# Kernel optimization log

Hardware: AMD Instinct MI355X
Metric: run time of the kernel (lower is better)

Reference implementation:

```python
import jax, jax.numpy as jnp
import numpy as np

B, T, D, H = 8, 8192, 1024, 16
HD = D // H  # head_dim = 64


def setup_inputs() -> dict:
    key = jax.random.key(0)
    ks = jax.random.split(key, 6)
    x = jax.random.normal(ks[0], (B, D), jnp.float32)
    past_k = jax.random.normal(ks[1], (B, T, H, HD), jnp.float32)
    past_v = jax.random.normal(ks[2], (B, T, H, HD), jnp.float32)
    idx = jax.random.randint(ks[3], (B,), 0, T)
    W_attn = jax.random.normal(ks[4], (D, 3 * D), jnp.float32) * 0.02
    b_attn = jnp.zeros((3 * D,), jnp.float32)
    W_proj = jax.random.normal(ks[5], (D, D), jnp.float32) * 0.02
    b_proj = jnp.zeros((D,), jnp.float32)
    return dict(x=x, past_k=past_k, past_v=past_v, idx=idx,
                W_attn=W_attn, b_attn=b_attn, W_proj=W_proj, b_proj=b_proj)


def reference(x, past_k, past_v, idx, W_attn, b_attn, W_proj, b_proj):
    # fused qkv projection: [B, 3D]
    qkv = x @ W_attn + b_attn
    q, k, v = jnp.split(qkv, 3, axis=-1)
    q = q.reshape(B, 1, H, HD)          # q_len = 1 (decode step)
    k_step = k.reshape(B, H, HD)
    v_step = v.reshape(B, H, HD)
    # one-hot scatter update of KV cache at position idx (as in original)
    oh = jax.nn.one_hot(idx, T, dtype=x.dtype)[:, :, None, None]  # [B,T,1,1]
    k_all = past_k * (1.0 - oh) + oh * k_step[:, None]            # [B,T,H,HD]
    v_all = past_v * (1.0 - oh) + oh * v_step[:, None]
    # causal mask over cache: positions <= idx are valid
    mask = jnp.arange(T) <= idx[:, None]                          # [B,T]
    scale = 1.0 / jnp.sqrt(jnp.asarray(HD, x.dtype))
    scores = jnp.einsum('bqhd,bkhd->bhqk', q * scale, k_all)      # [B,H,1,T]
    big_neg = jnp.finfo(scores.dtype).min
    scores = jnp.where(mask[:, None, None, :], scores, big_neg)
    attn = jax.nn.softmax(scores, axis=-1)
    y = jnp.einsum('bhqk,bkhd->bqhd', attn, v_all).reshape(B, D)
    y = y @ W_proj + b_proj
    return (y, k_step, v_step)
```

## Files before the change

kernel.cpp:

```cpp
#include <hip/hip_runtime.h>
#include <hip/hip_bf16.h>

#define BB 8
#define TT 8192
#define HH 16
#define HDIM 64
#define DDIM 1024
#define NS 16
#define TSPLIT 512
#define KS1 16
#define KS2 32

__device__ __forceinline__ int load_idx(const int* __restrict__ idx, int b) {
  const bool wide = (idx[1] == 0) && (idx[3] == 0) && (idx[5] == 0) && (idx[7] == 0);
  int v = wide ? idx[2 * b] : idx[b];
  return min(max(v, 0), TT - 1);
}

__global__ __launch_bounds__(256) void qkv_split_kernel(
    const float* __restrict__ x, const float* __restrict__ W,
    float* __restrict__ part)
{
  const int bid = blockIdx.x;
  const int ks = bid & (KS1 - 1);
  const int jc = (bid >> 4) % 3;
  const int b  = bid / (3 * KS1);
  const int tid = threadIdx.x;

  __shared__ float x_s[64];
  if (tid < 64) x_s[tid] = x[b * DDIM + ks * 64 + tid];
  __syncthreads();

  const int j0 = jc * 1024 + tid * 4;
  const float* wp = W + (size_t)(ks * 64) * 3072 + j0;
  float4 acc = {0.f, 0.f, 0.f, 0.f};
  #pragma unroll 8
  for (int dd = 0; dd < 64; ++dd) {
    float4 w4 = *(const float4*)(wp + (size_t)dd * 3072);
    const float xv = x_s[dd];
    acc.x += xv * w4.x; acc.y += xv * w4.y;
    acc.z += xv * w4.z; acc.w += xv * w4.w;
  }
  *(float4*)(part + (size_t)ks * (BB * 3072) + b * 3072 + j0) = acc;
}

__global__ __launch_bounds__(256) void qkv_reduce_kernel(
    const float* __restrict__ part, const float* __restrict__ bias,
    float* __restrict__ q_ws, float* __restrict__ kstep_ws,
    float* __restrict__ vstep_ws, float* __restrict__ out)
{
  const int g = blockIdx.x * 256 + threadIdx.x;
  const int b = g / 3072;
  const int j = g % 3072;
  float acc = bias[j];
  #pragma unroll
  for (int ks = 0; ks < KS1; ++ks) acc += part[(size_t)ks * (BB * 3072) + g];

  if (j < 1024) {
    q_ws[b * DDIM + j] = acc * 0.125f;
  } else if (j < 2048) {
    const int jj = j - 1024;
    kstep_ws[b * DDIM + jj] = acc;
    out[8192 + b * DDIM + jj] = acc;
  } else {
    const int jj = j - 2048;
    vstep_ws[b * DDIM + jj] = acc;
    out[16384 + b * DDIM + jj] = acc;
  }
}

__global__ __launch_bounds__(256) void attn_partial_kernel(
    const float* __restrict__ past_k, const float* __restrict__ past_v,
    const int* __restrict__ idx,
    const float* __restrict__ q_ws, const float* __restrict__ kstep_ws,
    const float* __restrict__ vstep_ws,
    float* __restrict__ part_m, float* __restrict__ part_l,
    float* __restrict__ part_o)
{
  const int tid = threadIdx.x;
  const int s  = blockIdx.x & (NS - 1);
  const int h  = (blockIdx.x >> 4) & (HH - 1);
  const int b  = blockIdx.x >> 8;
  const int idxb = load_idx(idx, b);
  const int t0 = s * TSPLIT;
  const int bhs = (b * HH + h) * NS + s;

  if (t0 > idxb) {
    if (tid == 0) { part_m[bhs] = -1e30f; part_l[bhs] = 0.f; }
    return;
  }
  const int nvalid = min(TSPLIT, idxb - t0 + 1);

  __shared__ float q_s[HDIM];
  __shared__ float p_s[TSPLIT];
  __shared__ float redm[8], redl[8];
  __shared__ float o_s[16 * HDIM];

  if (tid < HDIM) q_s[tid] = q_ws[b * DDIM + h * HDIM + tid];
  __syncthreads();

  const float* Kb = past_k + (((size_t)b * TT + t0) * HH + h) * HDIM;
  const float* krow_step = kstep_ws + b * DDIM + h * HDIM;
  float sc[2];
  #pragma unroll
  for (int i = 0; i < 2; ++i) {
    const int tl = tid + i * 256;
    float v = -1e30f;
    if (tl < nvalid) {
      const float* kr = (t0 + tl == idxb) ? krow_step
                                          : (Kb + (size_t)tl * (HH * HDIM));
      const float4* k4 = (const float4*)kr;
      float a0 = 0.f, a1 = 0.f, a2 = 0.f, a3 = 0.f;
      #pragma unroll
      for (int seg = 0; seg < 16; ++seg) {
        float4 u = k4[seg];
        a0 += q_s[seg * 4 + 0] * u.x;
        a1 += q_s[seg * 4 + 1] * u.y;
        a2 += q_s[seg * 4 + 2] * u.z;
        a3 += q_s[seg * 4 + 3] * u.w;
      }
      v = (a0 + a1) + (a2 + a3);
    }
    sc[i] = v;
  }

  float lmax = fmaxf(sc[0], sc[1]);
  #pragma unroll
  for (int m = 32; m > 0; m >>= 1) lmax = fmaxf(lmax, __shfl_xor(lmax, m, 64));
  if ((tid & 63) == 0) redm[tid >> 6] = lmax;
  __syncthreads();
  const float mh = fmaxf(fmaxf(redm[0], redm[1]), fmaxf(redm[2], redm[3]));

  float lsum = 0.f;
  #pragma unroll
  for (int i = 0; i < 2; ++i) {
    float p = __expf(sc[i] - mh);
    p_s[tid + i * 256] = p;
    lsum += p;
  }
  #pragma unroll
  for (int m = 32; m > 0; m >>= 1) lsum += __shfl_xor(lsum, m, 64);
  if ((tid & 63) == 0) redl[tid >> 6] = lsum;
  __syncthreads();
  if (tid == 0) {
    part_m[bhs] = mh;
    part_l[bhs] = redl[0] + redl[1] + redl[2] + redl[3];
  }

  const int tg = tid >> 4;
  const int d0 = (tid & 15) * 4;
  const float* Vb = past_v + (((size_t)b * TT + t0) * HH + h) * HDIM + d0;
  const float* vrow_step = vstep_ws + b * DDIM + h * HDIM + d0;
  float a0 = 0.f, a1 = 0.f, a2 = 0.f, a3 = 0.f;
  for (int tl = tg; tl < nvalid; tl += 16) {
    const float p = p_s[tl];
    const float4 u = *(const float4*)((t0 + tl == idxb)
                                          ? vrow_step
                                          : (Vb + (size_t)tl * (HH * HDIM)));
    a0 += p * u.x; a1 += p * u.y; a2 += p * u.z; a3 += p * u.w;
  }
  o_s[tg * HDIM + d0 + 0] = a0;
  o_s[tg * HDIM + d0 + 1] = a1;
  o_s[tg * HDIM + d0 + 2] = a2;
  o_s[tg * HDIM + d0 + 3] = a3;
  __syncthreads();
  if (tid < HDIM) {
    float acc = 0.f;
    #pragma unroll
    for (int g2 = 0; g2 < 16; ++g2) acc += o_s[g2 * HDIM + tid];
    part_o[(size_t)bhs * HDIM + tid] = acc;
  }
}

__global__ __launch_bounds__(64) void attn_combine_kernel(
    const float* __restrict__ part_m, const float* __restrict__ part_l,
    const float* __restrict__ part_o, float* __restrict__ y_ws)
{
  const int bh = blockIdx.x;
  const int lane = threadIdx.x;

  float m[NS], l[NS];
  float M = -1e30f;
  #pragma unroll
  for (int s = 0; s < NS; ++s) {
    m[s] = part_m[bh * NS + s];
    l[s] = part_l[bh * NS + s];
    M = fmaxf(M, m[s]);
  }
  float L = 0.f, acc = 0.f;
  #pragma unroll
  for (int s = 0; s < NS; ++s) {
    float w = (l[s] > 0.f) ? __expf(m[s] - M) : 0.f;
    if (w > 0.f) {
      L += l[s] * w;
      acc += w * part_o[(size_t)(bh * NS + s) * HDIM + lane];
    }
  }
  y_ws[bh * HDIM + lane] = (L > 0.f) ? (acc / L) : 0.f;
}

__global__ __launch_bounds__(256) void proj_split_kernel(
    const float* __restrict__ y_ws, const float* __restrict__ W,
    float* __restrict__ part)
{
  const int bid = blockIdx.x;
  const int ks = bid & (KS2 - 1);
  const int b  = bid >> 5;
  const int tid = threadIdx.x;

  __shared__ float y_s[32];
  if (tid < 32) y_s[tid] = y_ws[b * DDIM + ks * 32 + tid];
  __syncthreads();

  const int j0 = tid * 4;
  const float* wp = W + (size_t)(ks * 32) * DDIM + j0;
  float4 acc = {0.f, 0.f, 0.f, 0.f};
  #pragma unroll 8
  for (int dd = 0; dd < 32; ++dd) {
    float4 w4 = *(const float4*)(wp + (size_t)dd * DDIM);
    const float yv = y_s[dd];
    acc.x += yv * w4.x; acc.y += yv * w4.y;
    acc.z += yv * w4.z; acc.w += yv * w4.w;
  }
  *(float4*)(part + (size_t)ks * (BB * DDIM) + b * DDIM + j0) = acc;
}

__global__ __launch_bounds__(256) void proj_reduce_kernel(
    const float* __restrict__ part, const float* __restrict__ bias,
    float* __restrict__ out)
{
  const int g = blockIdx.x * 256 + threadIdx.x;
  const int j = g & 1023;
  float acc = bias[j];
  #pragma unroll
  for (int ks = 0; ks < KS2; ++ks) acc += part[(size_t)ks * (BB * DDIM) + g];
  out[g] = acc;
}

extern "C" void kernel_launch(void* const* d_in, const int* in_sizes, int n_in,
                              void* d_out, int out_size, void* d_ws, size_t ws_size,
                              hipStream_t stream) {
  const float* x      = (const float*)d_in[0];
  const float* past_k = (const float*)d_in[1];
  const float* past_v = (const float*)d_in[2];
  const int*   idx    = (const int*)  d_in[3];
  const float* W_attn = (const float*)d_in[4];
  const float* b_attn = (const float*)d_in[5];
  const float* W_proj = (const float*)d_in[6];
  const float* b_proj = (const float*)d_in[7];
  float* out = (float*)d_out;

  float* ws        = (float*)d_ws;
  float* q_ws      = ws;
  float* kstep_ws  = ws + 8192;
  float* vstep_ws  = ws + 16384;
  float* y_ws      = ws + 24576;
  float* part_m    = ws + 32768;
  float* part_l    = ws + 34816;
  float* part_o    = ws + 36864;
  float* qkv_part  = ws + 167936;
  float* proj_part = ws + 561152;

  qkv_split_kernel<<<dim3(BB * 3 * KS1), dim3(256), 0, stream>>>(
      x, W_attn, qkv_part);
  qkv_reduce_kernel<<<dim3(96), dim3(256), 0, stream>>>(
      qkv_part, b_attn, q_ws, kstep_ws, vstep_ws, out);
  attn_partial_kernel<<<dim3(BB * HH * NS), dim3(256), 0, stream>>>(
      past_k, past_v, idx, q_ws, kstep_ws, vstep_ws, part_m, part_l, part_o);
  attn_combine_kernel<<<dim3(BB * HH), dim3(64), 0, stream>>>(
      part_m, part_l, part_o, y_ws);
  proj_split_kernel<<<dim3(BB * KS2), dim3(256), 0, stream>>>(
      y_ws, W_proj, proj_part);
  proj_reduce_kernel<<<dim3(32), dim3(256), 0, stream>>>(
      proj_part, b_proj, out);
}
```

Baseline: 540.2 us.

## Coalesce K dot-products across lanes, fuse attention combine into projection, double QKV split

The score computation now gives four lanes to each key row, each loading interleaved float4 chunks, and reduces them with lane shuffles. This makes global K reads more coalesced than the previous one-row-per-thread pattern. The separate attention-combine kernel is removed and its log-sum-exp merge is recomputed inside the projection split kernel, saving one launch at the cost of redundant combine work across blocks. The QKV split factor is doubled so more blocks read W_attn in parallel, which doubles the partial-sum traffic in the reduce kernel.

```diff
diff --git a/kernel.cpp b/kernel.cpp
--- a/kernel.cpp
+++ b/kernel.cpp
@@ -8,7 +8,7 @@
 #define DDIM 1024
 #define NS 16
 #define TSPLIT 512
-#define KS1 16
+#define KS1 32
 #define KS2 32
 
 __device__ __forceinline__ int load_idx(const int* __restrict__ idx, int b) {
@@ -23,19 +23,19 @@
 {
   const int bid = blockIdx.x;
   const int ks = bid & (KS1 - 1);
-  const int jc = (bid >> 4) % 3;
+  const int jc = (bid >> 5) % 3;
   const int b  = bid / (3 * KS1);
   const int tid = threadIdx.x;
 
-  __shared__ float x_s[64];
-  if (tid < 64) x_s[tid] = x[b * DDIM + ks * 64 + tid];
+  __shared__ float x_s[32];
+  if (tid < 32) x_s[tid] = x[b * DDIM + ks * 32 + tid];
   __syncthreads();
 
   const int j0 = jc * 1024 + tid * 4;
-  const float* wp = W + (size_t)(ks * 64) * 3072 + j0;
+  const float* wp = W + (size_t)(ks * 32) * 3072 + j0;
   float4 acc = {0.f, 0.f, 0.f, 0.f};
   #pragma unroll 8
-  for (int dd = 0; dd < 64; ++dd) {
+  for (int dd = 0; dd < 32; ++dd) {
     float4 w4 = *(const float4*)(wp + (size_t)dd * 3072);
     const float xv = x_s[dd];
     acc.x += xv * w4.x; acc.y += xv * w4.y;
@@ -101,43 +101,50 @@
 
   const float* Kb = past_k + (((size_t)b * TT + t0) * HH + h) * HDIM;
   const float* krow_step = kstep_ws + b * DDIM + h * HDIM;
-  float sc[2];
-  #pragma unroll
-  for (int i = 0; i < 2; ++i) {
-    const int tl = tid + i * 256;
-    float v = -1e30f;
-    if (tl < nvalid) {
-      const float* kr = (t0 + tl == idxb) ? krow_step
-                                          : (Kb + (size_t)tl * (HH * HDIM));
+  const int rowg = tid >> 2;
+  const int li   = tid & 3;
+  #pragma unroll
+  for (int r = 0; r < 8; ++r) {
+    const int row = rowg + r * 64;
+    float a = 0.f;
+    if (row < nvalid) {
+      const float* kr = (t0 + row == idxb)
+                            ? krow_step
+                            : (Kb + (size_t)row * (HH * HDIM));
       const float4* k4 = (const float4*)kr;
       float a0 = 0.f, a1 = 0.f, a2 = 0.f, a3 = 0.f;
       #pragma unroll
-      for (int seg = 0; seg < 16; ++seg) {
-        float4 u = k4[seg];
-        a0 += q_s[seg * 4 + 0] * u.x;
-        a1 += q_s[seg * 4 + 1] * u.y;
-        a2 += q_s[seg * 4 + 2] * u.z;
-        a3 += q_s[seg * 4 + 3] * u.w;
+      for (int i = 0; i < 4; ++i) {
+        const int q4 = li + i * 4;
+        float4 u = k4[q4];
+        const int d = q4 * 4;
+        a0 += q_s[d + 0] * u.x;
+        a1 += q_s[d + 1] * u.y;
+        a2 += q_s[d + 2] * u.z;
+        a3 += q_s[d + 3] * u.w;
       }
-      v = (a0 + a1) + (a2 + a3);
+      a = (a0 + a1) + (a2 + a3);
     }
-    sc[i] = v;
-  }
-
-  float lmax = fmaxf(sc[0], sc[1]);
+    a += __shfl_xor(a, 1, 64);
+    a += __shfl_xor(a, 2, 64);
+    if (li == 0) p_s[row] = (row < nvalid) ? a : -1e30f;
+  }
+  __syncthreads();
+
+  const float s0 = p_s[tid];
+  const float s1 = p_s[tid + 256];
+  float lmax = fmaxf(s0, s1);
   #pragma unroll
   for (int m = 32; m > 0; m >>= 1) lmax = fmaxf(lmax, __shfl_xor(lmax, m, 64));
   if ((tid & 63) == 0) redm[tid >> 6] = lmax;
   __syncthreads();
   const float mh = fmaxf(fmaxf(redm[0], redm[1]), fmaxf(redm[2], redm[3]));
 
-  float lsum = 0.f;
-  #pragma unroll
-  for (int i = 0; i < 2; ++i) {
-    float p = __expf(sc[i] - mh);
-    p_s[tid + i * 256] = p;
-    lsum += p;
-  }
+  const float p0 = __expf(s0 - mh);
+  const float p1 = __expf(s1 - mh);
+  p_s[tid] = p0;
+  p_s[tid + 256] = p1;
+  float lsum = p0 + p1;
   #pragma unroll
   for (int m = 32; m > 0; m >>= 1) lsum += __shfl_xor(lsum, m, 64);
   if ((tid & 63) == 0) redl[tid >> 6] = lsum;
@@ -172,36 +179,10 @@
   }
 }
 
-__global__ __launch_bounds__(64) void attn_combine_kernel(
+__global__ __launch_bounds__(256) void proj_split_kernel(
     const float* __restrict__ part_m, const float* __restrict__ part_l,
-    const float* __restrict__ part_o, float* __restrict__ y_ws)
-{
-  const int bh = blockIdx.x;
-  const int lane = threadIdx.x;
-
-  float m[NS], l[NS];
-  float M = -1e30f;
-  #pragma unroll
-  for (int s = 0; s < NS; ++s) {
-    m[s] = part_m[bh * NS + s];
-    l[s] = part_l[bh * NS + s];
-    M = fmaxf(M, m[s]);
-  }
-  float L = 0.f, acc = 0.f;
-  #pragma unroll
-  for (int s = 0; s < NS; ++s) {
-    float w = (l[s] > 0.f) ? __expf(m[s] - M) : 0.f;
-    if (w > 0.f) {
-      L += l[s] * w;
-      acc += w * part_o[(size_t)(bh * NS + s) * HDIM + lane];
-    }
-  }
-  y_ws[bh * HDIM + lane] = (L > 0.f) ? (acc / L) : 0.f;
-}
-
-__global__ __launch_bounds__(256) void proj_split_kernel(
-    const float* __restrict__ y_ws, const float* __restrict__ W,
-    float* __restrict__ part)
+    const float* __restrict__ part_o,
+    const float* __restrict__ W, float* __restrict__ part)
 {
   const int bid = blockIdx.x;
   const int ks = bid & (KS2 - 1);
@@ -209,7 +190,29 @@
   const int tid = threadIdx.x;
 
   __shared__ float y_s[32];
-  if (tid < 32) y_s[tid] = y_ws[b * DDIM + ks * 32 + tid];
+  if (tid < 32) {
+    const int h = ks >> 1;
+    const int d = (ks & 1) * 32 + tid;
+    const int bh = b * HH + h;
+    float m[NS], l[NS];
+    float M = -1e30f;
+    #pragma unroll
+    for (int s = 0; s < NS; ++s) {
+      m[s] = part_m[bh * NS + s];
+      l[s] = part_l[bh * NS + s];
+      M = fmaxf(M, m[s]);
+    }
+    float L = 0.f, acc = 0.f;
+    #pragma unroll
+    for (int s = 0; s < NS; ++s) {
+      float w = (l[s] > 0.f) ? __expf(m[s] - M) : 0.f;
+      if (w > 0.f) {
+        L += l[s] * w;
+        acc += w * part_o[(size_t)(bh * NS + s) * HDIM + d];
+      }
+    }
+    y_s[tid] = (L > 0.f) ? (acc / L) : 0.f;
+  }
   __syncthreads();
 
   const int j0 = tid * 4;
@@ -254,12 +257,11 @@
   float* q_ws      = ws;
   float* kstep_ws  = ws + 8192;
   float* vstep_ws  = ws + 16384;
-  float* y_ws      = ws + 24576;
-  float* part_m    = ws + 32768;
-  float* part_l    = ws + 34816;
-  float* part_o    = ws + 36864;
-  float* qkv_part  = ws + 167936;
-  float* proj_part = ws + 561152;
+  float* part_m    = ws + 24576;
+  float* part_l    = ws + 26624;
+  float* part_o    = ws + 28672;
+  float* qkv_part  = ws + 159744;
+  float* proj_part = ws + 946176;
 
   qkv_split_kernel<<<dim3(BB * 3 * KS1), dim3(256), 0, stream>>>(
       x, W_attn, qkv_part);
@@ -267,10 +269,8 @@
       qkv_part, b_attn, q_ws, kstep_ws, vstep_ws, out);
   attn_partial_kernel<<<dim3(BB * HH * NS), dim3(256), 0, stream>>>(
       past_k, past_v, idx, q_ws, kstep_ws, vstep_ws, part_m, part_l, part_o);
-  attn_combine_kernel<<<dim3(BB * HH), dim3(64), 0, stream>>>(
-      part_m, part_l, part_o, y_ws);
   proj_split_kernel<<<dim3(BB * KS2), dim3(256), 0, stream>>>(
-      y_ws, W_proj, proj_part);
+      part_m, part_l, part_o, W_proj, proj_part);
   proj_reduce_kernel<<<dim3(32), dim3(256), 0, stream>>>(
       proj_part, b_proj, out);
 }
```

After: 510.3 us. 1.06x faster.
